# Performance work log

Hardware: AMD Instinct MI355X
Metric: run time of the kernel (lower is better)

## Reference

```python
import jax, jax.numpy as jnp
import numpy as np

B, S, D, H = 4, 2048, 1024, 16
DH = D // H  # 64


def setup_inputs() -> dict:
    key = jax.random.key(0)
    ks = jax.random.split(key, 8)
    sc = 1.0 / np.sqrt(D)
    return {
        "hidden_states": jax.random.normal(ks[0], (B, S, D), jnp.float32),
        "attention_mask": jnp.zeros((B, 1, 1, S), jnp.float32),
        "Wq": jax.random.normal(ks[1], (D, D), jnp.float32) * sc,
        "bq": jnp.zeros((D,), jnp.float32),
        "Wk": jax.random.normal(ks[2], (D, D), jnp.float32) * sc,
        "bk": jnp.zeros((D,), jnp.float32),
        "Wv": jax.random.normal(ks[3], (D, D), jnp.float32) * sc,
        "bv": jnp.zeros((D,), jnp.float32),
    }


def _heads(x):
    # [B,S,D] -> [B,H,S,DH]
    b, s, _ = x.shape
    return x.reshape(b, s, H, DH).transpose(0, 2, 1, 3)


def reference(hidden_states, attention_mask, Wq, bq, Wk, bk, Wv, bv):
    q = _heads(hidden_states @ Wq + bq)
    k = _heads(hidden_states @ Wk + bk)
    v = _heads(hidden_states @ Wv + bv)
    scores = jnp.einsum('bhqd,bhkd->bhqk', q, k) / jnp.sqrt(jnp.float32(DH))
    scores = scores + attention_mask  # additive mask, broadcast
    probs = jax.nn.softmax(scores, axis=-1)  # dropout is identity in eval
    out = jnp.einsum('bhqk,bhkd->bhqd', probs, v)
    b, h, s, dh = out.shape
    return out.transpose(0, 2, 1, 3).reshape(b, s, h * dh)
```

## Files before the change

### kernel.cpp

```cpp
#include <hip/hip_runtime.h>
#include <hip/hip_bf16.h>
#include <cstdint>

typedef _Float16 f16;
typedef f16 f16x8 __attribute__((ext_vector_type(8)));
typedef f16 f16x4 __attribute__((ext_vector_type(4)));
typedef float f32x4 __attribute__((ext_vector_type(4)));

#define MFMA16(a, b, c) __builtin_amdgcn_mfma_f32_16x16x32_f16((a), (b), (c), 0, 0, 0)

constexpr int Bc = 4, Sc = 2048, Dc = 1024, Hc = 16, DHc = 64;

typedef __attribute__((address_space(1))) const uint32_t gbl_u32;
typedef __attribute__((address_space(3))) uint32_t lds_u32;
__device__ __forceinline__ void gld_lds16(const void* g, void* l) {
  __builtin_amdgcn_global_load_lds((gbl_u32*)g, (lds_u32*)l, 16, 0, 0);
}

__global__ __launch_bounds__(256) void cast_w_kernel(
    const float* __restrict__ Wq, const float* __restrict__ Wk,
    const float* __restrict__ Wv, f16* __restrict__ Wt) {
  __shared__ __align__(16) f16 T[64][66];
  const int z = blockIdx.z;
  const float* W = (z == 0) ? Wq : (z == 1) ? Wk : Wv;
  const int n0 = blockIdx.x * 64, k0 = blockIdx.y * 64;
  const int t = threadIdx.x;
#pragma unroll
  for (int p = 0; p < 4; p++) {
    int idx = t + p * 256;
    int r = idx >> 4, c = idx & 15;
    float4 v = *(const float4*)(W + (size_t)(k0 + r) * Dc + n0 + c * 4);
    T[r][c * 4 + 0] = (f16)v.x;
    T[r][c * 4 + 1] = (f16)v.y;
    T[r][c * 4 + 2] = (f16)v.z;
    T[r][c * 4 + 3] = (f16)v.w;
  }
  __syncthreads();
#pragma unroll
  for (int p = 0; p < 2; p++) {
    int idx = t + p * 256;
    int n = idx >> 3, c = idx & 7;
    f16x8 tmp;
#pragma unroll
    for (int j = 0; j < 8; j++) tmp[j] = T[c * 8 + j][n];
    *(f16x8*)(Wt + ((size_t)z * Dc + n0 + n) * Dc + k0 + c * 8) = tmp;
  }
}

__global__ __launch_bounds__(256) void cast_x_kernel(const float* __restrict__ X,
                                                     f16* __restrict__ X16) {
  size_t i = ((size_t)blockIdx.x * 256 + threadIdx.x) * 8;
  float4 a = *(const float4*)(X + i);
  float4 b = *(const float4*)(X + i + 4);
  f16x8 h;
  h[0] = (f16)a.x; h[1] = (f16)a.y; h[2] = (f16)a.z; h[3] = (f16)a.w;
  h[4] = (f16)b.x; h[5] = (f16)b.y; h[6] = (f16)b.z; h[7] = (f16)b.w;
  *(f16x8*)(X16 + i) = h;
}

__global__ __launch_bounds__(256) void qkv_gemm_kernel(
    const f16* __restrict__ X16, const f16* __restrict__ Wt,
    const float* __restrict__ bq, const float* __restrict__ bk,
    const float* __restrict__ bv, f16* __restrict__ Qo, f16* __restrict__ Ko,
    f16* __restrict__ Vo) {
  const int z = blockIdx.z;
  const f16* W = Wt + (size_t)z * Dc * Dc;
  const float* bias = (z == 0) ? bq : (z == 1) ? bk : bv;

  const int n0 = blockIdx.x * 128, m0 = blockIdx.y * 128;
  __shared__ __align__(16) f16 Xs[128 * 32];
  __shared__ __align__(16) f16 Ws[128 * 32];

  const int t = threadIdx.x;
  const int wave = t >> 6, lane = t & 63;
  const int l16 = lane & 15, quad = lane >> 4;
  const int wm = (wave >> 1) * 64, wn = (wave & 1) * 64;

  f32x4 acc[4][4];
#pragma unroll
  for (int i = 0; i < 4; i++)
#pragma unroll
    for (int j = 0; j < 4; j++) acc[i][j] = (f32x4){0.f, 0.f, 0.f, 0.f};

  for (int k0 = 0; k0 < Dc; k0 += 32) {
#pragma unroll
    for (int p = 0; p < 2; p++) {
      int cb = p * 256 + wave * 64;
      int chunk = cb + lane;
      int row = chunk >> 2, c8 = (chunk & 3) * 8;
      gld_lds16(X16 + (size_t)(m0 + row) * Dc + k0 + c8, (f16*)Xs + (size_t)cb * 8);
      gld_lds16(W + (size_t)(n0 + row) * Dc + k0 + c8, (f16*)Ws + (size_t)cb * 8);
    }
    __syncthreads();

    f16x8 aF[4], bF[4];
#pragma unroll
    for (int mt = 0; mt < 4; mt++)
      aF[mt] = *(const f16x8*)(&Xs[(wm + mt * 16 + l16) * 32 + quad * 8]);
#pragma unroll
    for (int nt = 0; nt < 4; nt++)
      bF[nt] = *(const f16x8*)(&Ws[(wn + nt * 16 + l16) * 32 + quad * 8]);
#pragma unroll
    for (int mt = 0; mt < 4; mt++)
#pragma unroll
      for (int nt = 0; nt < 4; nt++)
        acc[mt][nt] = MFMA16(aF[mt], bF[nt], acc[mt][nt]);
    __syncthreads();
  }

#pragma unroll
  for (int nt = 0; nt < 4; nt++) {
    int col = n0 + wn + nt * 16 + l16;
    float bval = bias[col];
    int h = col >> 6, d = col & 63;
    if (z == 2) {
#pragma unroll
      for (int mt = 0; mt < 4; mt++) {
        int m = m0 + wm + mt * 16 + quad * 4;
        int b = m >> 11, sbase = m & 2047;
        f16x4 pk;
#pragma unroll
        for (int r = 0; r < 4; r++) pk[r] = (f16)(acc[mt][nt][r] + bval);
        *(f16x4*)(Vo + (((size_t)(b * Hc + h)) * DHc + d) * Sc + sbase) = pk;
      }
    } else {
      const float sc = (z == 0) ? 0.125f : 1.0f;
      f16* O = (z == 0) ? Qo : Ko;
#pragma unroll
      for (int mt = 0; mt < 4; mt++) {
#pragma unroll
        for (int r = 0; r < 4; r++) {
          int m = m0 + wm + mt * 16 + quad * 4 + r;
          int b = m >> 11, s = m & 2047;
          O[(((size_t)(b * Hc + h)) * Sc + s) * DHc + d] =
              (f16)((acc[mt][nt][r] + bval) * sc);
        }
      }
    }
  }
}

__global__ __launch_bounds__(256) void flash_kernel(
    const f16* __restrict__ Q, const f16* __restrict__ K,
    const f16* __restrict__ Vt, const float* __restrict__ mask,
    float* __restrict__ out) {
  const int bh = blockIdx.y;
  const int b = bh >> 4, h = bh & 15;
  const int t = threadIdx.x;
  const int wave = t >> 6, lane = t & 63;
  const int l16 = lane & 15, quad = lane >> 4;
  const int qbase = blockIdx.x * 64 + wave * 16;

  __shared__ __align__(16) f16 Ks[2][4096];
  __shared__ __align__(16) f16 Vs[2][4096];
  __shared__ __align__(16) float Ms[2048];
  __shared__ __align__(16) f16 Pbuf[4][16][76];

  const f16* Kb = K + (size_t)bh * Sc * DHc;
  const f16* Vb = Vt + (size_t)bh * DHc * Sc;
  const float* mrow = mask + (size_t)b * Sc;

  auto stageKV = [&](int c0, int buf) {
#pragma unroll
    for (int p = 0; p < 2; p++) {
      int cb = p * 256 + wave * 64;
      int i = cb + lane;
      int half = i >> 8, row = (i >> 2) & 63, q8 = i & 3;
      gld_lds16(Kb + (size_t)(c0 + row) * DHc + half * 32 + q8 * 8,
                &Ks[buf][cb * 8]);
      gld_lds16(Vb + (size_t)row * Sc + c0 + half * 32 + q8 * 8,
                &Vs[buf][cb * 8]);
    }
  };

  f16x8 qa0, qa1;
  {
    const f16* qb = Q + ((size_t)bh * Sc + qbase + l16) * DHc;
    qa0 = *(const f16x8*)(qb + quad * 8);
    qa1 = *(const f16x8*)(qb + 32 + quad * 8);
  }

  stageKV(0, 0);
#pragma unroll
  for (int p = 0; p < 2; p++) {
    int cb = p * 256 + wave * 64;
    gld_lds16(mrow + (size_t)(cb + lane) * 4, &Ms[cb * 4]);
  }
  __syncthreads();

  float l_acc = 0.f;
  f32x4 o[4];
#pragma unroll
  for (int dt = 0; dt < 4; dt++) o[dt] = (f32x4){0.f, 0.f, 0.f, 0.f};

  for (int c = 0; c < 32; c++) {
    const int buf = c & 1;
    if (c < 31) stageKV((c + 1) * 64, buf ^ 1);

    f16x8 ka[4][2];
#pragma unroll
    for (int nt = 0; nt < 4; nt++) {
      ka[nt][0] = *(const f16x8*)(&Ks[buf][(nt * 16 + l16) * 32 + quad * 8]);
      ka[nt][1] =
          *(const f16x8*)(&Ks[buf][2048 + (nt * 16 + l16) * 32 + quad * 8]);
    }
    float4 mv[4];
#pragma unroll
    for (int nt = 0; nt < 4; nt++)
      mv[nt] = *(const float4*)(&Ms[c * 64 + nt * 16 + quad * 4]);

    float ls = 0.f;
#pragma unroll
    for (int nt = 0; nt < 4; nt++) {
      f32x4 a = (f32x4){mv[nt].x, mv[nt].y, mv[nt].z, mv[nt].w};
      a = MFMA16(ka[nt][0], qa0, a);
      a = MFMA16(ka[nt][1], qa1, a);
      f16x4 pk;
#pragma unroll
      for (int r = 0; r < 4; r++) {
        float p = __expf(a[r]);
        ls += p;
        pk[r] = (f16)p;
      }
      *(f16x4*)(&Pbuf[wave][l16][nt * 16 + quad * 4]) = pk;
    }
    l_acc += ls;

    const f16* prow = &Pbuf[wave][l16][0];
    f16x4 a0 = *(const f16x4*)(prow + quad * 8);
    f16x4 a1 = *(const f16x4*)(prow + quad * 8 + 4);
    f16x4 b0 = *(const f16x4*)(prow + 32 + quad * 8);
    f16x4 b1 = *(const f16x4*)(prow + 32 + quad * 8 + 4);
    f16x8 pa0 = __builtin_shufflevector(a0, a1, 0, 1, 2, 3, 4, 5, 6, 7);
    f16x8 pa1 = __builtin_shufflevector(b0, b1, 0, 1, 2, 3, 4, 5, 6, 7);

#pragma unroll
    for (int dt = 0; dt < 4; dt++) {
      f16x8 v0 = *(const f16x8*)(&Vs[buf][(dt * 16 + l16) * 32 + quad * 8]);
      f16x8 v1 =
          *(const f16x8*)(&Vs[buf][2048 + (dt * 16 + l16) * 32 + quad * 8]);
      o[dt] = MFMA16(pa0, v0, o[dt]);
      o[dt] = MFMA16(pa1, v1, o[dt]);
    }

    __syncthreads();
  }

  l_acc += __shfl_xor(l_acc, 16);
  l_acc += __shfl_xor(l_acc, 32);
  float inv[4];
#pragma unroll
  for (int r = 0; r < 4; r++) inv[r] = 1.0f / __shfl(l_acc, quad * 4 + r);
#pragma unroll
  for (int dt = 0; dt < 4; dt++) {
    int col = h * 64 + dt * 16 + l16;
#pragma unroll
    for (int r = 0; r < 4; r++) {
      int row = qbase + quad * 4 + r;
      out[((size_t)b * Sc + row) * Dc + col] = o[dt][r] * inv[r];
    }
  }
}

extern "C" void kernel_launch(void* const* d_in, const int* in_sizes, int n_in,
                              void* d_out, int out_size, void* d_ws,
                              size_t ws_size, hipStream_t stream) {
  (void)in_sizes; (void)n_in; (void)out_size; (void)ws_size;
  const float* hidden = (const float*)d_in[0];
  const float* mask   = (const float*)d_in[1];
  const float* Wq     = (const float*)d_in[2];
  const float* bq     = (const float*)d_in[3];
  const float* Wk     = (const float*)d_in[4];
  const float* bk     = (const float*)d_in[5];
  const float* Wv     = (const float*)d_in[6];
  const float* bv     = (const float*)d_in[7];
  float* out = (float*)d_out;

  uint8_t* w = (uint8_t*)d_ws;
  f16* Wt   = (f16*)(w);
  f16* X16  = (f16*)(w + (size_t)6 * 1024 * 1024);
  f16* Q16  = (f16*)(w + (size_t)22 * 1024 * 1024);
  f16* K16  = (f16*)(w + (size_t)38 * 1024 * 1024);
  f16* Vt16 = (f16*)(w + (size_t)54 * 1024 * 1024);

  cast_w_kernel<<<dim3(16, 16, 3), 256, 0, stream>>>(Wq, Wk, Wv, Wt);
  cast_x_kernel<<<4096, 256, 0, stream>>>(hidden, X16);
  qkv_gemm_kernel<<<dim3(8, 64, 3), 256, 0, stream>>>(X16, Wt, bq, bk, bv,
                                                      Q16, K16, Vt16);
  flash_kernel<<<dim3(32, 64), 256, 0, stream>>>(Q16, K16, Vt16, mask, out);
}
```

Baseline: 308.1 us.

## Process two query tiles per wave in flash kernel with XOR-swizzled K/V LDS

Each wave now handles 32 query rows (two 16-row tiles) instead of 16, so every K and V tile staged into LDS is reused twice and the grid is halved. The softmax and exp of the first tile is interleaved with the QK MFMAs of the second tile to overlap ALU work with matrix work. K/V LDS layout gets an XOR swizzle on 16-byte chunks to reduce bank conflicts on fragment reads. The cost is higher register pressure (two sets of accumulators) and half as many blocks, which may lower occupancy or leave CUs underused.

Result: faster. 287.2 us (-6.8%).

```diff
diff --git a/kernel.cpp b/kernel.cpp
--- a/kernel.cpp
+++ b/kernel.cpp
@@ -149,7 +149,7 @@
   const int t = threadIdx.x;
   const int wave = t >> 6, lane = t & 63;
   const int l16 = lane & 15, quad = lane >> 4;
-  const int qbase = blockIdx.x * 64 + wave * 16;
+  const int qbase = blockIdx.x * 128 + wave * 32;
 
   __shared__ __align__(16) f16 Ks[2][4096];
   __shared__ __align__(16) f16 Vs[2][4096];
@@ -160,24 +160,28 @@
   const f16* Vb = Vt + (size_t)bh * DHc * Sc;
   const float* mrow = mask + (size_t)b * Sc;
 
+  const int qsw8 = (quad ^ ((l16 >> 1) & 3)) * 8;
+
   auto stageKV = [&](int c0, int buf) {
 #pragma unroll
     for (int p = 0; p < 2; p++) {
       int cb = p * 256 + wave * 64;
       int i = cb + lane;
       int half = i >> 8, row = (i >> 2) & 63, q8 = i & 3;
-      gld_lds16(Kb + (size_t)(c0 + row) * DHc + half * 32 + q8 * 8,
+      int q8g = q8 ^ ((row >> 1) & 3);
+      gld_lds16(Kb + (size_t)(c0 + row) * DHc + half * 32 + q8g * 8,
                 &Ks[buf][cb * 8]);
-      gld_lds16(Vb + (size_t)row * Sc + c0 + half * 32 + q8 * 8,
+      gld_lds16(Vb + (size_t)row * Sc + c0 + half * 32 + q8g * 8,
                 &Vs[buf][cb * 8]);
     }
   };
 
-  f16x8 qa0, qa1;
-  {
-    const f16* qb = Q + ((size_t)bh * Sc + qbase + l16) * DHc;
-    qa0 = *(const f16x8*)(qb + quad * 8);
-    qa1 = *(const f16x8*)(qb + 32 + quad * 8);
+  f16x8 qa[2][2];
+#pragma unroll
+  for (int mt = 0; mt < 2; mt++) {
+    const f16* qb = Q + ((size_t)bh * Sc + qbase + mt * 16 + l16) * DHc;
+    qa[mt][0] = *(const f16x8*)(qb + quad * 8);
+    qa[mt][1] = *(const f16x8*)(qb + 32 + quad * 8);
   }
 
   stageKV(0, 0);
@@ -188,10 +192,12 @@
   }
   __syncthreads();
 
-  float l_acc = 0.f;
-  f32x4 o[4];
-#pragma unroll
-  for (int dt = 0; dt < 4; dt++) o[dt] = (f32x4){0.f, 0.f, 0.f, 0.f};
+  float l_acc[2] = {0.f, 0.f};
+  f32x4 o[2][4];
+#pragma unroll
+  for (int mt = 0; mt < 2; mt++)
+#pragma unroll
+    for (int dt = 0; dt < 4; dt++) o[mt][dt] = (f32x4){0.f, 0.f, 0.f, 0.f};
 
   for (int c = 0; c < 32; c++) {
     const int buf = c & 1;
@@ -200,64 +206,123 @@
     f16x8 ka[4][2];
 #pragma unroll
     for (int nt = 0; nt < 4; nt++) {
-      ka[nt][0] = *(const f16x8*)(&Ks[buf][(nt * 16 + l16) * 32 + quad * 8]);
-      ka[nt][1] =
-          *(const f16x8*)(&Ks[buf][2048 + (nt * 16 + l16) * 32 + quad * 8]);
+      int rb = (nt * 16 + l16) * 32 + qsw8;
+      ka[nt][0] = *(const f16x8*)(&Ks[buf][rb]);
+      ka[nt][1] = *(const f16x8*)(&Ks[buf][2048 + rb]);
     }
     float4 mv[4];
 #pragma unroll
     for (int nt = 0; nt < 4; nt++)
       mv[nt] = *(const float4*)(&Ms[c * 64 + nt * 16 + quad * 4]);
 
-    float ls = 0.f;
+    f32x4 s0[4];
 #pragma unroll
     for (int nt = 0; nt < 4; nt++) {
       f32x4 a = (f32x4){mv[nt].x, mv[nt].y, mv[nt].z, mv[nt].w};
-      a = MFMA16(ka[nt][0], qa0, a);
-      a = MFMA16(ka[nt][1], qa1, a);
-      f16x4 pk;
+      a = MFMA16(ka[nt][0], qa[0][0], a);
+      a = MFMA16(ka[nt][1], qa[0][1], a);
+      s0[nt] = a;
+    }
+    {
+      float ls = 0.f;
+#pragma unroll
+      for (int nt = 0; nt < 4; nt++) {
+        f16x4 pk;
+#pragma unroll
+        for (int r = 0; r < 4; r++) {
+          float p = __expf(s0[nt][r]);
+          ls += p;
+          pk[r] = (f16)p;
+        }
+        *(f16x4*)(&Pbuf[wave][l16][nt * 16 + quad * 4]) = pk;
+      }
+      l_acc[0] += ls;
+    }
+
+    f32x4 s1[4];
+#pragma unroll
+    for (int nt = 0; nt < 4; nt++) {
+      f32x4 a = (f32x4){mv[nt].x, mv[nt].y, mv[nt].z, mv[nt].w};
+      a = MFMA16(ka[nt][0], qa[1][0], a);
+      a = MFMA16(ka[nt][1], qa[1][1], a);
+      s1[nt] = a;
+    }
+
+    f16x8 pa0, pa1;
+    {
+      const f16* prow = &Pbuf[wave][l16][0];
+      f16x4 a0 = *(const f16x4*)(prow + quad * 8);
+      f16x4 a1 = *(const f16x4*)(prow + quad * 8 + 4);
+      f16x4 b0 = *(const f16x4*)(prow + 32 + quad * 8);
+      f16x4 b1 = *(const f16x4*)(prow + 32 + quad * 8 + 4);
+      pa0 = __builtin_shufflevector(a0, a1, 0, 1, 2, 3, 4, 5, 6, 7);
+      pa1 = __builtin_shufflevector(b0, b1, 0, 1, 2, 3, 4, 5, 6, 7);
+    }
+    f16x8 vb[4][2];
+#pragma unroll
+    for (int dt = 0; dt < 4; dt++) {
+      int rb = (dt * 16 + l16) * 32 + qsw8;
+      vb[dt][0] = *(const f16x8*)(&Vs[buf][rb]);
+      vb[dt][1] = *(const f16x8*)(&Vs[buf][2048 + rb]);
+    }
+#pragma unroll
+    for (int dt = 0; dt < 4; dt++) {
+      o[0][dt] = MFMA16(pa0, vb[dt][0], o[0][dt]);
+      o[0][dt] = MFMA16(pa1, vb[dt][1], o[0][dt]);
+    }
+
+    {
+      float ls = 0.f;
+#pragma unroll
+      for (int nt = 0; nt < 4; nt++) {
+        f16x4 pk;
+#pragma unroll
+        for (int r = 0; r < 4; r++) {
+          float p = __expf(s1[nt][r]);
+          ls += p;
+          pk[r] = (f16)p;
+        }
+        *(f16x4*)(&Pbuf[wave][l16][nt * 16 + quad * 4]) = pk;
+      }
+      l_acc[1] += ls;
+    }
+    {
+      const f16* prow = &Pbuf[wave][l16][0];
+      f16x4 a0 = *(const f16x4*)(prow + quad * 8);
+      f16x4 a1 = *(const f16x4*)(prow + quad * 8 + 4);
+      f16x4 b0 = *(const f16x4*)(prow + 32 + quad * 8);
+      f16x4 b1 = *(const f16x4*)(prow + 32 + quad * 8 + 4);
+      f16x8 qa0p = __builtin_shufflevector(a0, a1, 0, 1, 2, 3, 4, 5, 6, 7);
+      f16x8 qa1p = __builtin_shufflevector(b0, b1, 0, 1, 2, 3, 4, 5, 6, 7);
+#pragma unroll
+      for (int dt = 0; dt < 4; dt++) {
+        o[1][dt] = MFMA16(qa0p, vb[dt][0], o[1][dt]);
+        o[1][dt] = MFMA16(qa1p, vb[dt][1], o[1][dt]);
+      }
+    }
+
+    __syncthreads();
+  }
+
+#pragma unroll
+  for (int mt = 0; mt < 2; mt++) {
+    l_acc[mt] += __shfl_xor(l_acc[mt], 16);
+    l_acc[mt] += __shfl_xor(l_acc[mt], 32);
+  }
+#pragma unroll
+  for (int mt = 0; mt < 2; mt++) {
+    float inv[4];
+#pragma unroll
+    for (int r = 0; r < 4; r++)
+      inv[r] = 1.0f / __shfl(l_acc[mt], quad * 4 + r);
+#pragma unroll
+    for (int dt = 0; dt < 4; dt++) {
+      int col = h * 64 + dt * 16 + l16;
 #pragma unroll
       for (int r = 0; r < 4; r++) {
-        float p = __expf(a[r]);
-        ls += p;
-        pk[r] = (f16)p;
-      }
-      *(f16x4*)(&Pbuf[wave][l16][nt * 16 + quad * 4]) = pk;
-    }
-    l_acc += ls;
-
-    const f16* prow = &Pbuf[wave][l16][0];
-    f16x4 a0 = *(const f16x4*)(prow + quad * 8);
-    f16x4 a1 = *(const f16x4*)(prow + quad * 8 + 4);
-    f16x4 b0 = *(const f16x4*)(prow + 32 + quad * 8);
-    f16x4 b1 = *(const f16x4*)(prow + 32 + quad * 8 + 4);
-    f16x8 pa0 = __builtin_shufflevector(a0, a1, 0, 1, 2, 3, 4, 5, 6, 7);
-    f16x8 pa1 = __builtin_shufflevector(b0, b1, 0, 1, 2, 3, 4, 5, 6, 7);
-
-#pragma unroll
-    for (int dt = 0; dt < 4; dt++) {
-      f16x8 v0 = *(const f16x8*)(&Vs[buf][(dt * 16 + l16) * 32 + quad * 8]);
-      f16x8 v1 =
-          *(const f16x8*)(&Vs[buf][2048 + (dt * 16 + l16) * 32 + quad * 8]);
-      o[dt] = MFMA16(pa0, v0, o[dt]);
-      o[dt] = MFMA16(pa1, v1, o[dt]);
-    }
-
-    __syncthreads();
-  }
-
-  l_acc += __shfl_xor(l_acc, 16);
-  l_acc += __shfl_xor(l_acc, 32);
-  float inv[4];
-#pragma unroll
-  for (int r = 0; r < 4; r++) inv[r] = 1.0f / __shfl(l_acc, quad * 4 + r);
-#pragma unroll
-  for (int dt = 0; dt < 4; dt++) {
-    int col = h * 64 + dt * 16 + l16;
-#pragma unroll
-    for (int r = 0; r < 4; r++) {
-      int row = qbase + quad * 4 + r;
-      out[((size_t)b * Sc + row) * Dc + col] = o[dt][r] * inv[r];
+        int row = qbase + mt * 16 + quad * 4 + r;
+        out[((size_t)b * Sc + row) * Dc + col] = o[mt][dt][r] * inv[r];
+      }
     }
   }
 }
@@ -287,5 +352,5 @@
   cast_x_kernel<<<4096, 256, 0, stream>>>(hidden, X16);
   qkv_gemm_kernel<<<dim3(8, 64, 3), 256, 0, stream>>>(X16, Wt, bq, bk, bv,
                                                       Q16, K16, Vt16);
-  flash_kernel<<<dim3(32, 64), 256, 0, stream>>>(Q16, K16, Vt16, mask, out);
-}
+  flash_kernel<<<dim3(16, 64), 256, 0, stream>>>(Q16, K16, Vt16, mask, out);
+}
```
